# Performance work log

Hardware: AMD Instinct MI355X
Metric: run time of the kernel (lower is better)

Reference implementation:

```python
import jax, jax.numpy as jnp
import numpy as np

B, S, D = 4, 2048, 1024
MAG_SCALE = 5.0


def setup_inputs() -> dict:
    key = jax.random.key(0)
    ks = jax.random.split(key, 16)
    sd = 1.0 / np.sqrt(D)  # keep pre-activations O(1)
    inp = {
        "x": jax.random.normal(ks[0], (B, S, D), jnp.float32),
        "W_omega": jax.random.normal(ks[1], (D, D), jnp.float32) * sd,
        "b_omega": jnp.zeros((D,), jnp.float32),
        "W_mag": jax.random.normal(ks[2], (D, D), jnp.float32) * sd,
        "b_mag": jnp.zeros((D,), jnp.float32),
        "W_phi0": jax.random.normal(ks[3], (D, D), jnp.float32) * sd,
        "b_phi0": jnp.zeros((D,), jnp.float32),
        "W_gate": jax.random.normal(ks[4], (D, D), jnp.float32) * sd,
        "b_gate": jnp.zeros((D,), jnp.float32),
        "W_q": jax.random.normal(ks[5], (D, D), jnp.float32) * sd,
        "b_q": jnp.zeros((D,), jnp.float32),
        "integration_scale": jax.random.uniform(ks[6], (D,), jnp.float32),
        "W_out": jax.random.normal(ks[7], (4 * D, D), jnp.float32) * (1.0 / np.sqrt(4 * D)),
        "b_out": jnp.zeros((D,), jnp.float32),
    }
    return inp


def reference(x, W_omega, b_omega, W_mag, b_mag, W_phi0, b_phi0,
              W_gate, b_gate, W_q, b_q, integration_scale, W_out, b_out):
    lin = lambda h, W, b: h @ W + b  # [B,S,*] @ [*,Dout]

    omega = lin(x, W_omega, b_omega)                      # phase velocity [B,S,D]
    magnitude = jax.nn.sigmoid(lin(x, W_mag, b_mag)) * MAG_SCALE
    gate = jax.nn.sigmoid(lin(x, W_gate, b_gate))
    gated_omega = gate * (omega * jnp.abs(integration_scale))
    phi = lin(x, W_phi0, b_phi0) + jnp.cumsum(gated_omega, axis=1)  # integrated phase

    cos_phi = jnp.cos(phi)
    sin_phi = jnp.sin(phi)

    # holographic memory write: cumulative complex binding of content with phase
    weighted_content = magnitude * x
    memory_real = jnp.cumsum(weighted_content * cos_phi, axis=1)
    memory_imag = jnp.cumsum(weighted_content * sin_phi, axis=1)
    sqrt_mag = jnp.sqrt(jnp.cumsum(magnitude, axis=1) + 1e-8)
    memory_real = memory_real / sqrt_mag
    memory_imag = memory_imag / sqrt_mag

    # complex retrieval at a query phase
    phi_q = phi + lin(x, W_q, b_q)
    cos_q, sin_q = jnp.cos(phi_q), jnp.sin(phi_q)
    retrieved_real = memory_real * cos_q + memory_imag * sin_q
    retrieved_imag = memory_imag * cos_q - memory_real * sin_q

    context = jnp.concatenate(
        [x * cos_phi, x * sin_phi, retrieved_real, retrieved_imag], axis=-1)  # [B,S,4D]
    return x + lin(context, W_out, b_out)


if __name__ == "__main__":
    out = reference(**setup_inputs())
    print(out.shape, out.dtype)
```

## Files before the change

kernel.cpp:

```cpp
#include <hip/hip_runtime.h>
#include <hip/hip_fp16.h>

#define B_ 4
#define S_ 2048
#define D_ 1024
#define CCH 64
#define LCH 32
#define NELEM ((size_t)B_*S_*D_)
#define MROWS (B_*S_)

typedef __attribute__((ext_vector_type(16))) float f32x16;
typedef __attribute__((ext_vector_type(8))) _Float16 f16x8;

__device__ __forceinline__ ushort f2h(float v) {
  __half h = __float2half(v);
  return __builtin_bit_cast(ushort, h);
}
__device__ __forceinline__ float h2f(ushort u) {
  return __half2float(__builtin_bit_cast(__half, u));
}

__device__ __forceinline__ void gload16(const ushort* src, char* ldsdst) {
  __builtin_amdgcn_global_load_lds(
      (const __attribute__((address_space(1))) void*)src,
      (__attribute__((address_space(3))) void*)ldsdst, 16, 0, 0);
}


__global__ void xhalf_kernel(const float* __restrict__ x, ushort* __restrict__ xh) {
  size_t i = ((size_t)blockIdx.x * blockDim.x + threadIdx.x) * 8;
  if (i >= NELEM) return;
  float4 a = *(const float4*)(x + i);
  float4 b = *(const float4*)(x + i + 4);
  ushort h[8] = {f2h(a.x), f2h(a.y), f2h(a.z), f2h(a.w),
                 f2h(b.x), f2h(b.y), f2h(b.z), f2h(b.w)};
  *(ushort4*)(xh + i) = *(ushort4*)h;
  *(ushort4*)(xh + i + 4) = *(ushort4*)(h + 4);
}

__global__ void transpose_convert(const float* __restrict__ W, ushort* __restrict__ Th, int sh,
                                  int Kd, int Nd) {
  __shared__ float tile[64][65];
  const int k0 = blockIdx.x * 64, n0 = blockIdx.y * 64;
  const int tx = threadIdx.x & 63, ty = threadIdx.x >> 6;
#pragma unroll
  for (int i = 0; i < 16; ++i)
    tile[ty * 16 + i][tx] = W[(size_t)(k0 + ty * 16 + i) * Nd + n0 + tx];
  __syncthreads();
#pragma unroll
  for (int i = 0; i < 16; ++i) {
    const int nn = ty * 16 + i;
    Th[(size_t)(n0 + nn) * sh + k0 + tx] = f2h(tile[tx][nn]);
  }
}

template <int FINAL, int SPLITK>
__global__ __launch_bounds__(512, 2) void gemm256(
    const ushort* __restrict__ A, int lda, const ushort* __restrict__ Bw,
    ushort* __restrict__ Ch, ushort* __restrict__ C4h,
    float* __restrict__ Cf, float* __restrict__ C4f,
    const float* __restrict__ xres, const float* __restrict__ bias,
    int M, int K) {
  __shared__ __align__(16) char ldsc[2 * 32768];
  int bid = blockIdx.x, ks = 0;
  if (SPLITK && bid >= 128) { ks = 1; bid -= 128; }
  const int tm = bid & 31, tn = bid >> 5;
  const int Kb = SPLITK ? (K >> 1) : K;
  const int ldb = K;
  const int nB = tn << 8;
  if (SPLITK) { A += (size_t)ks * Kb; Bw += (size_t)ks * Kb; }
  const int NT = Kb >> 5;
  const int t = threadIdx.x, lane = t & 63, wid = t >> 6;
  const int wm = wid >> 2, wn = wid & 3;

  f32x16 acc[4][2];
#pragma unroll
  for (int i = 0; i < 4; ++i)
#pragma unroll
    for (int j = 0; j < 2; ++j)
#pragma unroll
      for (int r = 0; r < 16; ++r) acc[i][j][r] = 0.f;

  const int line1 = t >> 3;
  const int g8s = (t & 7) ^ (line1 & 7);
  const int rowS = line1 * 2 + (g8s >> 2);
  const int kgS = (g8s & 3) << 3;
  const ushort* srcA = A + (size_t)(tm * 256 + rowS) * lda + kgS;
  const ushort* srcB = Bw + (size_t)(nB + rowS) * ldb + kgS;
  char* dstA = ldsc + (size_t)t * 16;
  char* dstB = ldsc + 16384 + (size_t)t * 16;

  auto STAGE = [&](int tile) {
    if (tile >= NT) return;
    char* ba = dstA + (tile & 1) * 32768;
    char* bb = dstB + (tile & 1) * 32768;
    const ushort* sa = srcA + tile * 32;
    const ushort* sb = srcB + tile * 32;
    gload16(sa, ba);
    gload16(sa + (size_t)128 * lda, ba + 8192);
    gload16(sb, bb);
    gload16(sb + (size_t)128 * ldb, bb + 8192);
  };

  const int l31 = lane & 31;
  const int lline = l31 >> 1;
  const int lpar4 = (lane & 1) << 2;
  const int khi = lane >> 5;
  const int swzk0 = ((lpar4 + 0 + khi) ^ (lline & 7)) << 4;
  const int swzk1 = ((lpar4 + 2 + khi) ^ (lline & 7)) << 4;
  const char* aB = ldsc + wm * 8192 + lline * 128;
  const char* bB = ldsc + 16384 + wn * 4096 + lline * 128;

  STAGE(0);
  asm volatile("s_waitcnt vmcnt(0)" ::: "memory");
  __builtin_amdgcn_sched_barrier(0);
  __builtin_amdgcn_s_barrier();

#pragma unroll 1
  for (int tt = 0; tt < NT; ++tt) {
    STAGE(tt + 1);
    const char* ab = aB + (tt & 1) * 32768;
    const char* bb = bB + (tt & 1) * 32768;
    f16x8 af[4][2], bf_[2][2];
#pragma unroll
    for (int mt = 0; mt < 4; ++mt) af[mt][0] = *(const f16x8*)(ab + mt * 2048 + swzk0);
#pragma unroll
    for (int nt = 0; nt < 2; ++nt) bf_[nt][0] = *(const f16x8*)(bb + nt * 2048 + swzk0);
#pragma unroll
    for (int mt = 0; mt < 4; ++mt) af[mt][1] = *(const f16x8*)(ab + mt * 2048 + swzk1);
#pragma unroll
    for (int nt = 0; nt < 2; ++nt) bf_[nt][1] = *(const f16x8*)(bb + nt * 2048 + swzk1);
    asm volatile("s_waitcnt lgkmcnt(6)" ::: "memory");
    __builtin_amdgcn_sched_barrier(0);
    __builtin_amdgcn_s_setprio(1);
#pragma unroll
    for (int mt = 0; mt < 4; ++mt)
#pragma unroll
      for (int nt = 0; nt < 2; ++nt)
        acc[mt][nt] = __builtin_amdgcn_mfma_f32_32x32x16_f16(af[mt][0], bf_[nt][0], acc[mt][nt], 0, 0, 0);
    __builtin_amdgcn_s_setprio(0);
    asm volatile("s_waitcnt lgkmcnt(0)" ::: "memory");
    __builtin_amdgcn_sched_barrier(0);
    __builtin_amdgcn_s_setprio(1);
#pragma unroll
    for (int mt = 0; mt < 4; ++mt)
#pragma unroll
      for (int nt = 0; nt < 2; ++nt)
        acc[mt][nt] = __builtin_amdgcn_mfma_f32_32x32x16_f16(af[mt][1], bf_[nt][1], acc[mt][nt], 0, 0, 0);
    __builtin_amdgcn_s_setprio(0);
    asm volatile("s_waitcnt vmcnt(0)" ::: "memory");
    __builtin_amdgcn_sched_barrier(0);
    __builtin_amdgcn_s_barrier();
  }

#pragma unroll
  for (int mt = 0; mt < 4; ++mt) {
    const int rowb = tm * 256 + wm * 128 + mt * 32 + 4 * khi;
#pragma unroll
    for (int nt = 0; nt < 2; ++nt) {
      const int col = tn * 256 + wn * 64 + nt * 32 + l31;
      if (SPLITK && ks) {
#pragma unroll
        for (int r = 0; r < 16; ++r) {
          const int row = rowb + (r & 3) + 8 * (r >> 2);
          C4f[(size_t)row * 1024 + col] = acc[mt][nt][r];
        }
      } else if (FINAL) {
#pragma unroll
        for (int r = 0; r < 16; ++r) {
          const int row = rowb + (r & 3) + 8 * (r >> 2);
          const size_t idx = (size_t)row * 1024 + col;
          Cf[idx] = acc[mt][nt][r] + xres[idx] + bias[col];
        }
      } else {
        const int pl = col >> 10;
        ushort* base = (pl < 4) ? (Ch + (size_t)pl * (size_t)M * 1024) : C4h;
#pragma unroll
        for (int r = 0; r < 16; ++r) {
          const int row = rowb + (r & 3) + 8 * (r >> 2);
          base[(size_t)row * 1024 + (col & 1023)] = f2h(acc[mt][nt][r]);
        }
      }
    }
  }
}

__global__ void add_kernel(float* __restrict__ out, const float* __restrict__ p) {
  size_t i = ((size_t)blockIdx.x * blockDim.x + threadIdx.x) * 4;
  if (i >= NELEM) return;
  float4 a = *(const float4*)(out + i);
  float4 b = *(const float4*)(p + i);
  a.x += b.x; a.y += b.y; a.z += b.z; a.w += b.w;
  *(float4*)(out + i) = a;
}


__device__ __forceinline__ void load4h(const ushort* p, float* f) {
  ushort4 u = *(const ushort4*)p;
  f[0] = h2f(u.x); f[1] = h2f(u.y); f[2] = h2f(u.z); f[3] = h2f(u.w);
}

__global__ void prep_chunk_kernel(ushort* __restrict__ omega_go, const ushort* __restrict__ gate_lin,
                                  ushort* __restrict__ mag_io,
                                  const float* __restrict__ b_om, const float* __restrict__ b_gate,
                                  const float* __restrict__ b_mag, const float* __restrict__ isc,
                                  float* __restrict__ gsum, float* __restrict__ msum) {
  int tid = blockIdx.x * blockDim.x + threadIdx.x;
  if (tid >= B_ * CCH * (D_ / 4)) return;
  int d4 = tid & 255, c = (tid >> 8) & (CCH - 1), b = tid >> 14;
  int d = d4 * 4;
  size_t base = ((size_t)(b * S_) + c * LCH) * D_ + d;
  size_t cs = ((size_t)(b * CCH) + c) * D_ + d;
  float bo[4], bg[4], bm[4], is[4];
  *(float4*)bo = *(const float4*)(b_om + d);
  *(float4*)bg = *(const float4*)(b_gate + d);
  *(float4*)bm = *(const float4*)(b_mag + d);
  *(float4*)is = *(const float4*)(isc + d);
  float sg[4] = {0.f, 0.f, 0.f, 0.f}, sm[4] = {0.f, 0.f, 0.f, 0.f};
  for (int s = 0; s < LCH; ++s) {
    size_t i = base + (size_t)s * D_;
    float om[4], gl[4], mg[4];
    load4h(omega_go + i, om);
    load4h(gate_lin + i, gl);
    load4h(mag_io + i, mg);
    ushort wo[4], wm_[4];
#pragma unroll
    for (int j = 0; j < 4; ++j) {
      float g = 1.f / (1.f + __expf(-(gl[j] + bg[j])));
      float m5 = 5.f / (1.f + __expf(-(mg[j] + bm[j])));
      float go = g * ((om[j] + bo[j]) * fabsf(is[j]));
      sg[j] += go;
      sm[j] += m5;
      wo[j] = f2h(go);
      wm_[j] = f2h(m5);
    }
    *(ushort4*)(omega_go + i) = *(ushort4*)wo;
    *(ushort4*)(mag_io + i) = *(ushort4*)wm_;
  }
  *(float4*)(gsum + cs) = *(float4*)sg;
  *(float4*)(msum + cs) = *(float4*)sm;
}

__global__ void scan_offsets_kernel(float* __restrict__ s1, float* __restrict__ s2) {
  int gw = (blockIdx.x * blockDim.x + threadIdx.x) >> 6;
  int lane = threadIdx.x & 63;
  if (gw >= B_ * D_) return;
  int d = gw & (D_ - 1), b = gw >> 10;
  size_t idx = ((size_t)(b * CCH) + lane) * D_ + d;
  float v1 = s1[idx], v2 = s2[idx];
#pragma unroll
  for (int off = 1; off < 64; off <<= 1) {
    float u1 = __shfl_up(v1, off);
    float u2 = __shfl_up(v2, off);
    if (lane >= off) { v1 += u1; v2 += u2; }
  }
  float e1 = __shfl_up(v1, 1), e2 = __shfl_up(v2, 1);
  if (lane == 0) { e1 = 0.f; e2 = 0.f; }
  s1[idx] = e1;
  s2[idx] = e2;
}

__global__ void phase_scan_kernel(const float* __restrict__ x, const ushort* __restrict__ go,
                                  const ushort* __restrict__ mag, const ushort* __restrict__ p0,
                                  const float* __restrict__ goff,
                                  float* __restrict__ trsum, float* __restrict__ tisum,
                                  const float* __restrict__ b_phi, ushort* __restrict__ ctx) {
  int tid = blockIdx.x * blockDim.x + threadIdx.x;
  if (tid >= B_ * CCH * (D_ / 4)) return;
  int d4 = tid & 255, c = (tid >> 8) & (CCH - 1), b = tid >> 14;
  int d = d4 * 4;
  size_t base = ((size_t)(b * S_) + c * LCH) * D_ + d;
  size_t cs = ((size_t)(b * CCH) + c) * D_ + d;
  float pr[4], bp[4];
  *(float4*)pr = *(const float4*)(goff + cs);
  *(float4*)bp = *(const float4*)(b_phi + d);
  float tr[4] = {0.f, 0.f, 0.f, 0.f}, ti[4] = {0.f, 0.f, 0.f, 0.f};
  size_t crow = ((size_t)(b * S_ + c * LCH)) * 4096 + d;
  for (int s = 0; s < LCH; ++s) {
    size_t i = base + (size_t)s * D_;
    float g[4], ph0[4], m[4], xv[4];
    load4h(go + i, g);
    load4h(p0 + i, ph0);
    load4h(mag + i, m);
    *(float4*)xv = *(const float4*)(x + i);
    ushort c4[4], s4[4];
#pragma unroll
    for (int j = 0; j < 4; ++j) {
      pr[j] += g[j];
      float ph = ph0[j] + bp[j] + pr[j];
      float sp, cp;
      __sincosf(ph, &sp, &cp);
      float wr = m[j] * xv[j];
      tr[j] += wr * cp;
      ti[j] += wr * sp;
      c4[j] = f2h(xv[j] * cp);
      s4[j] = f2h(xv[j] * sp);
    }
    *(ushort4*)(ctx + crow) = *(ushort4*)c4;
    *(ushort4*)(ctx + crow + 1024) = *(ushort4*)s4;
    crow += 4096;
  }
  *(float4*)(trsum + cs) = *(float4*)tr;
  *(float4*)(tisum + cs) = *(float4*)ti;
}

__global__ void retrieve_kernel(const float* __restrict__ x, const ushort* __restrict__ go,
                                const ushort* __restrict__ mag, const ushort* __restrict__ p0,
                                const ushort* __restrict__ q,
                                const float* __restrict__ goff, const float* __restrict__ moff,
                                const float* __restrict__ troff, const float* __restrict__ tioff,
                                const float* __restrict__ b_phi, const float* __restrict__ b_q,
                                ushort* __restrict__ ctx) {
  int tid = blockIdx.x * blockDim.x + threadIdx.x;
  if (tid >= B_ * CCH * (D_ / 4)) return;
  int d4 = tid & 255, c = (tid >> 8) & (CCH - 1), b = tid >> 14;
  int d = d4 * 4;
  size_t base = ((size_t)(b * S_) + c * LCH) * D_ + d;
  size_t cs = ((size_t)(b * CCH) + c) * D_ + d;
  float pr[4], mr[4], tr[4], ti[4], bp[4], bq[4];
  *(float4*)pr = *(const float4*)(goff + cs);
  *(float4*)mr = *(const float4*)(moff + cs);
  *(float4*)tr = *(const float4*)(troff + cs);
  *(float4*)ti = *(const float4*)(tioff + cs);
  *(float4*)bp = *(const float4*)(b_phi + d);
  *(float4*)bq = *(const float4*)(b_q + d);
  size_t crow = ((size_t)(b * S_ + c * LCH)) * 4096 + d;
  for (int s = 0; s < LCH; ++s) {
    size_t i = base + (size_t)s * D_;
    float g[4], ph0[4], m[4], xv[4], qv[4];
    load4h(go + i, g);
    load4h(p0 + i, ph0);
    load4h(mag + i, m);
    load4h(q + i, qv);
    *(float4*)xv = *(const float4*)(x + i);
    ushort r2[4], r3[4];
#pragma unroll
    for (int j = 0; j < 4; ++j) {
      pr[j] += g[j];
      float ph = ph0[j] + bp[j] + pr[j];
      float sp, cp;
      __sincosf(ph, &sp, &cp);
      mr[j] += m[j];
      float wr = m[j] * xv[j];
      tr[j] += wr * cp;
      ti[j] += wr * sp;
      float rs = rsqrtf(mr[j] + 1e-8f);
      float mreal = tr[j] * rs, mimag = ti[j] * rs;
      float phq = ph + qv[j] + bq[j];
      float sq, cq;
      __sincosf(phq, &sq, &cq);
      r2[j] = f2h(mreal * cq + mimag * sq);
      r3[j] = f2h(mimag * cq - mreal * sq);
    }
    *(ushort4*)(ctx + crow + 2048) = *(ushort4*)r2;
    *(ushort4*)(ctx + crow + 3072) = *(ushort4*)r3;
    crow += 4096;
  }
}

extern "C" void kernel_launch(void* const* d_in, const int* in_sizes, int n_in,
                              void* d_out, int out_size, void* d_ws, size_t ws_size,
                              hipStream_t stream) {
  const float* x      = (const float*)d_in[0];
  const float* W_om   = (const float*)d_in[1];
  const float* b_om   = (const float*)d_in[2];
  const float* W_mag  = (const float*)d_in[3];
  const float* b_mag  = (const float*)d_in[4];
  const float* W_phi  = (const float*)d_in[5];
  const float* b_phi  = (const float*)d_in[6];
  const float* W_gate = (const float*)d_in[7];
  const float* b_gate = (const float*)d_in[8];
  const float* W_q    = (const float*)d_in[9];
  const float* b_q    = (const float*)d_in[10];
  const float* isc    = (const float*)d_in[11];
  const float* W_out  = (const float*)d_in[12];
  const float* b_out  = (const float*)d_in[13];
  float* out = (float*)d_out;

  const size_t WS_NEEDED = 213909504ull;
  if (ws_size < WS_NEEDED) {
    (void)hipMemsetAsync(d_out, 0, (size_t)out_size * sizeof(float), stream);
    return;
  }
  char* w = (char*)d_ws;
  ushort* planes_h = (ushort*)w;
  ushort* omega_buf = planes_h;
  ushort* gate_buf  = planes_h + NELEM;
  ushort* mag_buf   = planes_h + 2 * NELEM;
  ushort* phi0_buf  = planes_h + 3 * NELEM;
  float* partial    = (float*)w;
  ushort* q_buf     = (ushort*)out;
  char* ctxb = w + 4 * NELEM * 4;
  ushort* ctx   = (ushort*)ctxb;
  ushort* x_h   = (ushort*)ctxb;
  ushort* W5T   = (ushort*)(ctxb + 16777216);
  ushort* WoutT = (ushort*)(w + 201326592);
  float* gsum  = (float*)(w + 209715200);
  float* msum  = (float*)(w + 210763776);
  float* trsum = (float*)(w + 211812352);
  float* tisum = (float*)(w + 212860928);

  const size_t DD = (size_t)D_ * D_;

  xhalf_kernel<<<(int)(NELEM / 2048), 256, 0, stream>>>(x, x_h);
  dim3 tg(16, 16);
  transpose_convert<<<tg, 256, 0, stream>>>(W_om,   W5T + 0 * DD, 1024, D_, D_);
  transpose_convert<<<tg, 256, 0, stream>>>(W_gate, W5T + 1 * DD, 1024, D_, D_);
  transpose_convert<<<tg, 256, 0, stream>>>(W_mag,  W5T + 2 * DD, 1024, D_, D_);
  transpose_convert<<<tg, 256, 0, stream>>>(W_phi,  W5T + 3 * DD, 1024, D_, D_);
  transpose_convert<<<tg, 256, 0, stream>>>(W_q,    W5T + 4 * DD, 1024, D_, D_);
  transpose_convert<<<dim3(64, 16), 256, 0, stream>>>(W_out, WoutT, 4096, 4 * D_, D_);

  gemm256<0, 0><<<640, 512, 0, stream>>>(x_h, 1024, W5T, planes_h, q_buf,
                                         nullptr, nullptr, nullptr, nullptr, MROWS, 1024);

  prep_chunk_kernel<<<B_ * CCH * (D_ / 4) / 256, 256, 0, stream>>>(
      omega_buf, gate_buf, mag_buf, b_om, b_gate, b_mag, isc, gsum, msum);
  scan_offsets_kernel<<<B_ * D_ * 64 / 256, 256, 0, stream>>>(gsum, msum);
  phase_scan_kernel<<<B_ * CCH * (D_ / 4) / 256, 256, 0, stream>>>(
      x, omega_buf, mag_buf, phi0_buf, gsum, trsum, tisum, b_phi, ctx);
  scan_offsets_kernel<<<B_ * D_ * 64 / 256, 256, 0, stream>>>(trsum, tisum);
  retrieve_kernel<<<B_ * CCH * (D_ / 4) / 256, 256, 0, stream>>>(
      x, omega_buf, mag_buf, phi0_buf, q_buf, gsum, msum, trsum, tisum, b_phi, b_q, ctx);

  gemm256<1, 1><<<256, 512, 0, stream>>>(ctx, 4096, WoutT, nullptr, nullptr, out, partial,
                                         x, b_out, MROWS, 4 * D_);
  add_kernel<<<(int)(NELEM / 1024), 256, 0, stream>>>(out, partial);
}
```

Measured before the change: 333.4 us.

## Switch GEMM to 16x16x32 MFMA, batch weight transposes, read half-precision x in scans

The GEMM inner loop moves from 32x32x16 MFMA tiles to 16x16x32 tiles. This changes the LDS fragment addressing, the accumulator layout and the epilogue indexing. The five square weight transposes are merged into one launch using blockIdx.z. The phase-scan and retrieve kernels now read x as fp16 from a relocated x_h buffer instead of fp32 x, which halves that read traffic but lowers the precision of x in the memory accumulation.

```diff
diff --git a/kernel.cpp b/kernel.cpp
--- a/kernel.cpp
+++ b/kernel.cpp
@@ -9,7 +9,7 @@
 #define NELEM ((size_t)B_*S_*D_)
 #define MROWS (B_*S_)
 
-typedef __attribute__((ext_vector_type(16))) float f32x16;
+typedef __attribute__((ext_vector_type(4))) float f32x4;
 typedef __attribute__((ext_vector_type(8))) _Float16 f16x8;
 
 __device__ __forceinline__ ushort f2h(float v) {
@@ -36,6 +36,26 @@
                  f2h(b.x), f2h(b.y), f2h(b.z), f2h(b.w)};
   *(ushort4*)(xh + i) = *(ushort4*)h;
   *(ushort4*)(xh + i + 4) = *(ushort4*)(h + 4);
+}
+
+__global__ void transpose5(const float* __restrict__ W0, const float* __restrict__ W1,
+                           const float* __restrict__ W2, const float* __restrict__ W3,
+                           const float* __restrict__ W4, ushort* __restrict__ Th) {
+  __shared__ float tile[64][65];
+  const int z = blockIdx.z;
+  const float* W = (z == 0) ? W0 : (z == 1) ? W1 : (z == 2) ? W2 : (z == 3) ? W3 : W4;
+  ushort* T = Th + (size_t)z * D_ * D_;
+  const int k0 = blockIdx.x * 64, n0 = blockIdx.y * 64;
+  const int tx = threadIdx.x & 63, ty = threadIdx.x >> 6;
+#pragma unroll
+  for (int i = 0; i < 16; ++i)
+    tile[ty * 16 + i][tx] = W[(size_t)(k0 + ty * 16 + i) * D_ + n0 + tx];
+  __syncthreads();
+#pragma unroll
+  for (int i = 0; i < 16; ++i) {
+    const int nn = ty * 16 + i;
+    T[(size_t)(n0 + nn) * D_ + k0 + tx] = f2h(tile[tx][nn]);
+  }
 }
 
 __global__ void transpose_convert(const float* __restrict__ W, ushort* __restrict__ Th, int sh,
@@ -73,13 +93,11 @@
   const int t = threadIdx.x, lane = t & 63, wid = t >> 6;
   const int wm = wid >> 2, wn = wid & 3;
 
-  f32x16 acc[4][2];
-#pragma unroll
-  for (int i = 0; i < 4; ++i)
-#pragma unroll
-    for (int j = 0; j < 2; ++j)
-#pragma unroll
-      for (int r = 0; r < 16; ++r) acc[i][j][r] = 0.f;
+  f32x4 acc[8][4];
+#pragma unroll
+  for (int i = 0; i < 8; ++i)
+#pragma unroll
+    for (int j = 0; j < 4; ++j) acc[i][j] = (f32x4){0.f, 0.f, 0.f, 0.f};
 
   const int line1 = t >> 3;
   const int g8s = (t & 7) ^ (line1 & 7);
@@ -102,14 +120,11 @@
     gload16(sb + (size_t)128 * ldb, bb + 8192);
   };
 
-  const int l31 = lane & 31;
-  const int lline = l31 >> 1;
-  const int lpar4 = (lane & 1) << 2;
-  const int khi = lane >> 5;
-  const int swzk0 = ((lpar4 + 0 + khi) ^ (lline & 7)) << 4;
-  const int swzk1 = ((lpar4 + 2 + khi) ^ (lline & 7)) << 4;
-  const char* aB = ldsc + wm * 8192 + lline * 128;
-  const char* bB = ldsc + 16384 + wn * 4096 + lline * 128;
+  const int lane15 = lane & 15;
+  const int hl = lane15 >> 1;
+  const int swz = ((((lane15 & 1) << 2) + (lane >> 4)) ^ hl) << 4;
+  const char* aB = ldsc + wm * 8192 + hl * 128 + swz;
+  const char* bB = ldsc + 16384 + wn * 4096 + hl * 128 + swz;
 
   STAGE(0);
   asm volatile("s_waitcnt vmcnt(0)" ::: "memory");
@@ -121,32 +136,30 @@
     STAGE(tt + 1);
     const char* ab = aB + (tt & 1) * 32768;
     const char* bb = bB + (tt & 1) * 32768;
-    f16x8 af[4][2], bf_[2][2];
-#pragma unroll
-    for (int mt = 0; mt < 4; ++mt) af[mt][0] = *(const f16x8*)(ab + mt * 2048 + swzk0);
-#pragma unroll
-    for (int nt = 0; nt < 2; ++nt) bf_[nt][0] = *(const f16x8*)(bb + nt * 2048 + swzk0);
-#pragma unroll
-    for (int mt = 0; mt < 4; ++mt) af[mt][1] = *(const f16x8*)(ab + mt * 2048 + swzk1);
-#pragma unroll
-    for (int nt = 0; nt < 2; ++nt) bf_[nt][1] = *(const f16x8*)(bb + nt * 2048 + swzk1);
-    asm volatile("s_waitcnt lgkmcnt(6)" ::: "memory");
+    f16x8 af[4], bf_[4], af2[4];
+#pragma unroll
+    for (int f = 0; f < 4; ++f) af[f] = *(const f16x8*)(ab + f * 1024);
+#pragma unroll
+    for (int c = 0; c < 4; ++c) bf_[c] = *(const f16x8*)(bb + c * 1024);
+#pragma unroll
+    for (int f = 0; f < 4; ++f) af2[f] = *(const f16x8*)(ab + 4096 + f * 1024);
+    asm volatile("s_waitcnt lgkmcnt(4)" ::: "memory");
     __builtin_amdgcn_sched_barrier(0);
     __builtin_amdgcn_s_setprio(1);
 #pragma unroll
-    for (int mt = 0; mt < 4; ++mt)
-#pragma unroll
-      for (int nt = 0; nt < 2; ++nt)
-        acc[mt][nt] = __builtin_amdgcn_mfma_f32_32x32x16_f16(af[mt][0], bf_[nt][0], acc[mt][nt], 0, 0, 0);
+    for (int f = 0; f < 4; ++f)
+#pragma unroll
+      for (int c = 0; c < 4; ++c)
+        acc[f][c] = __builtin_amdgcn_mfma_f32_16x16x32_f16(af[f], bf_[c], acc[f][c], 0, 0, 0);
     __builtin_amdgcn_s_setprio(0);
     asm volatile("s_waitcnt lgkmcnt(0)" ::: "memory");
     __builtin_amdgcn_sched_barrier(0);
     __builtin_amdgcn_s_setprio(1);
 #pragma unroll
-    for (int mt = 0; mt < 4; ++mt)
-#pragma unroll
-      for (int nt = 0; nt < 2; ++nt)
-        acc[mt][nt] = __builtin_amdgcn_mfma_f32_32x32x16_f16(af[mt][1], bf_[nt][1], acc[mt][nt], 0, 0, 0);
+    for (int f = 0; f < 4; ++f)
+#pragma unroll
+      for (int c = 0; c < 4; ++c)
+        acc[4 + f][c] = __builtin_amdgcn_mfma_f32_16x16x32_f16(af2[f], bf_[c], acc[4 + f][c], 0, 0, 0);
     __builtin_amdgcn_s_setprio(0);
     asm volatile("s_waitcnt vmcnt(0)" ::: "memory");
     __builtin_amdgcn_sched_barrier(0);
@@ -154,32 +167,27 @@
   }
 
 #pragma unroll
-  for (int mt = 0; mt < 4; ++mt) {
-    const int rowb = tm * 256 + wm * 128 + mt * 32 + 4 * khi;
-#pragma unroll
-    for (int nt = 0; nt < 2; ++nt) {
-      const int col = tn * 256 + wn * 64 + nt * 32 + l31;
+  for (int i = 0; i < 8; ++i) {
+    const int row0 = tm * 256 + wm * 128 + i * 16 + ((lane >> 4) << 2);
+#pragma unroll
+    for (int jj = 0; jj < 4; ++jj) {
+      const int col = tn * 256 + wn * 64 + jj * 16 + lane15;
       if (SPLITK && ks) {
 #pragma unroll
-        for (int r = 0; r < 16; ++r) {
-          const int row = rowb + (r & 3) + 8 * (r >> 2);
-          C4f[(size_t)row * 1024 + col] = acc[mt][nt][r];
-        }
+        for (int r = 0; r < 4; ++r)
+          C4f[(size_t)(row0 + r) * 1024 + col] = acc[i][jj][r];
       } else if (FINAL) {
 #pragma unroll
-        for (int r = 0; r < 16; ++r) {
-          const int row = rowb + (r & 3) + 8 * (r >> 2);
-          const size_t idx = (size_t)row * 1024 + col;
-          Cf[idx] = acc[mt][nt][r] + xres[idx] + bias[col];
+        for (int r = 0; r < 4; ++r) {
+          const size_t idx = (size_t)(row0 + r) * 1024 + col;
+          Cf[idx] = acc[i][jj][r] + xres[idx] + bias[col];
         }
       } else {
         const int pl = col >> 10;
         ushort* base = (pl < 4) ? (Ch + (size_t)pl * (size_t)M * 1024) : C4h;
 #pragma unroll
-        for (int r = 0; r < 16; ++r) {
-          const int row = rowb + (r & 3) + 8 * (r >> 2);
-          base[(size_t)row * 1024 + (col & 1023)] = f2h(acc[mt][nt][r]);
-        }
+        for (int r = 0; r < 4; ++r)
+          base[(size_t)(row0 + r) * 1024 + (col & 1023)] = f2h(acc[i][jj][r]);
       }
     }
   }
@@ -260,7 +268,7 @@
   s2[idx] = e2;
 }
 
-__global__ void phase_scan_kernel(const float* __restrict__ x, const ushort* __restrict__ go,
+__global__ void phase_scan_kernel(const ushort* __restrict__ xh, const ushort* __restrict__ go,
                                   const ushort* __restrict__ mag, const ushort* __restrict__ p0,
                                   const float* __restrict__ goff,
                                   float* __restrict__ trsum, float* __restrict__ tisum,
@@ -282,7 +290,7 @@
     load4h(go + i, g);
     load4h(p0 + i, ph0);
     load4h(mag + i, m);
-    *(float4*)xv = *(const float4*)(x + i);
+    load4h(xh + i, xv);
     ushort c4[4], s4[4];
 #pragma unroll
     for (int j = 0; j < 4; ++j) {
@@ -304,7 +312,7 @@
   *(float4*)(tisum + cs) = *(float4*)ti;
 }
 
-__global__ void retrieve_kernel(const float* __restrict__ x, const ushort* __restrict__ go,
+__global__ void retrieve_kernel(const ushort* __restrict__ xh, const ushort* __restrict__ go,
                                 const ushort* __restrict__ mag, const ushort* __restrict__ p0,
                                 const ushort* __restrict__ q,
                                 const float* __restrict__ goff, const float* __restrict__ moff,
@@ -332,7 +340,7 @@
     load4h(p0 + i, ph0);
     load4h(mag + i, m);
     load4h(q + i, qv);
-    *(float4*)xv = *(const float4*)(x + i);
+    load4h(xh + i, xv);
     ushort r2[4], r3[4];
 #pragma unroll
     for (int j = 0; j < 4; ++j) {
@@ -389,10 +397,10 @@
   ushort* mag_buf   = planes_h + 2 * NELEM;
   ushort* phi0_buf  = planes_h + 3 * NELEM;
   float* partial    = (float*)w;
-  ushort* q_buf     = (ushort*)out;
+  ushort* x_h   = (ushort*)(w + 67108864);
+  ushort* q_buf = (ushort*)out;
   char* ctxb = w + 4 * NELEM * 4;
   ushort* ctx   = (ushort*)ctxb;
-  ushort* x_h   = (ushort*)ctxb;
   ushort* W5T   = (ushort*)(ctxb + 16777216);
   ushort* WoutT = (ushort*)(w + 201326592);
   float* gsum  = (float*)(w + 209715200);
@@ -403,12 +411,7 @@
   const size_t DD = (size_t)D_ * D_;
 
   xhalf_kernel<<<(int)(NELEM / 2048), 256, 0, stream>>>(x, x_h);
-  dim3 tg(16, 16);
-  transpose_convert<<<tg, 256, 0, stream>>>(W_om,   W5T + 0 * DD, 1024, D_, D_);
-  transpose_convert<<<tg, 256, 0, stream>>>(W_gate, W5T + 1 * DD, 1024, D_, D_);
-  transpose_convert<<<tg, 256, 0, stream>>>(W_mag,  W5T + 2 * DD, 1024, D_, D_);
-  transpose_convert<<<tg, 256, 0, stream>>>(W_phi,  W5T + 3 * DD, 1024, D_, D_);
-  transpose_convert<<<tg, 256, 0, stream>>>(W_q,    W5T + 4 * DD, 1024, D_, D_);
+  transpose5<<<dim3(16, 16, 5), 256, 0, stream>>>(W_om, W_gate, W_mag, W_phi, W_q, W5T);
   transpose_convert<<<dim3(64, 16), 256, 0, stream>>>(W_out, WoutT, 4096, 4 * D_, D_);
 
   gemm256<0, 0><<<640, 512, 0, stream>>>(x_h, 1024, W5T, planes_h, q_buf,
@@ -418,10 +421,10 @@
       omega_buf, gate_buf, mag_buf, b_om, b_gate, b_mag, isc, gsum, msum);
   scan_offsets_kernel<<<B_ * D_ * 64 / 256, 256, 0, stream>>>(gsum, msum);
   phase_scan_kernel<<<B_ * CCH * (D_ / 4) / 256, 256, 0, stream>>>(
-      x, omega_buf, mag_buf, phi0_buf, gsum, trsum, tisum, b_phi, ctx);
+      x_h, omega_buf, mag_buf, phi0_buf, gsum, trsum, tisum, b_phi, ctx);
   scan_offsets_kernel<<<B_ * D_ * 64 / 256, 256, 0, stream>>>(trsum, tisum);
   retrieve_kernel<<<B_ * CCH * (D_ / 4) / 256, 256, 0, stream>>>(
-      x, omega_buf, mag_buf, phi0_buf, q_buf, gsum, msum, trsum, tisum, b_phi, b_q, ctx);
+      x_h, omega_buf, mag_buf, phi0_buf, q_buf, gsum, msum, trsum, tisum, b_phi, b_q, ctx);
 
   gemm256<1, 1><<<256, 512, 0, stream>>>(ctx, 4096, WoutT, nullptr, nullptr, out, partial,
                                          x, b_out, MROWS, 4 * D_);
```

Measured after the change: 318.4 us. -4.5%, faster.
